# Optimization experiments

Hardware: AMD Instinct MI355X
Metric: run time of the kernel (lower is better)

## Reference

```python
import jax, jax.numpy as jnp
import numpy as np
from jax.scipy.special import logsumexp

GRID_N = 512
N_ITERS = 5


def _build_grid(n):
    nH = n * (n - 1)
    E = 2 * n * (n - 1)
    P = (n - 1) * (n - 1)
    N = n * n
    pi, pj = np.meshgrid(np.arange(n - 1), np.arange(n - 1), indexing='ij')
    pi, pj = pi.ravel(), pj.ravel()
    # child edges of plaquette (i,j): top/bottom horizontal, left/right vertical
    pce = np.stack([pi * (n - 1) + pj,
                    (pi + 1) * (n - 1) + pj,
                    nH + pi * n + pj,
                    nH + pi * n + pj + 1], 1).astype(np.int32)
    epp = np.zeros((E, 2), np.int32)
    eps = np.zeros((E, 2), np.int32)
    epm = np.zeros((E, 2), np.float32)
    ev = np.zeros((E, 2), np.int32)
    hi, hj = np.meshgrid(np.arange(n), np.arange(n - 1), indexing='ij')
    hi, hj = hi.ravel(), hj.ravel()
    he = hi * (n - 1) + hj
    m = hi < n - 1
    epp[he[m], 0] = hi[m] * (n - 1) + hj[m]; epm[he[m], 0] = 1; eps[he, 0] = 0
    m = hi > 0
    epp[he[m], 1] = (hi[m] - 1) * (n - 1) + hj[m]; epm[he[m], 1] = 1; eps[he, 1] = 1
    ev[he, 0] = hi * n + hj; ev[he, 1] = hi * n + hj + 1
    vi, vj = np.meshgrid(np.arange(n - 1), np.arange(n), indexing='ij')
    vi, vj = vi.ravel(), vj.ravel()
    ve = nH + vi * n + vj
    m = vj < n - 1
    epp[ve[m], 0] = vi[m] * (n - 1) + vj[m]; epm[ve[m], 0] = 1; eps[ve, 0] = 2
    m = vj > 0
    epp[ve[m], 1] = vi[m] * (n - 1) + vj[m] - 1; epm[ve[m], 1] = 1; eps[ve, 1] = 3
    ev[ve, 0] = vi * n + vj; ev[ve, 1] = (vi + 1) * n + vj
    return epp, eps, epm, pce, ev, E, P, N


def setup_inputs() -> dict:
    n = GRID_N
    epp, eps, epm, pce, ev, E, P, N = _build_grid(n)
    key = jax.random.key(0)
    k1, k2 = jax.random.split(key)
    return {
        'log_phi_plaq': 0.5 * jax.random.normal(k1, (P, 2, 2, 2, 2), jnp.float32),
        'log_phi_edge': 0.5 * jax.random.normal(k2, (E, 2, 2), jnp.float32),
        'edge_parent_plaq': jnp.asarray(epp),
        'edge_parent_slot': jnp.asarray(eps),
        'edge_parent_mask': jnp.asarray(epm),
        'plaq_child_edge': jnp.asarray(pce),
        'edge_vars': jnp.asarray(ev),
        'n_iters': N_ITERS,
        'n_vars': N,
    }


def _forward(log_phi_plaq, log_phi_edge, epp, eps, epm, pce, ev, n_iters, n_vars):
    P = log_phi_plaq.shape[0]
    maskNN = epm[:, :, None, None]

    def edge_totals(logM):
        # sum of log-messages from (<=2) parents into each edge, plus edge factor
        g = logM[epp, eps]                      # [E,2,2,2]
        return log_phi_edge + jnp.sum(g * maskNN, axis=1)  # [E,2,2]

    def plaq_terms(logM, tot):
        n_all = tot[pce] - logM                 # [P,4,2,2]: child msg excluding this parent
        b0 = n_all[:, 0, :, :, None, None]      # top edge -> vars (a,b)
        b1 = n_all[:, 1, None, None, :, :]      # bottom  -> vars (c,d)
        b2 = n_all[:, 2, :, None, :, None]      # left    -> vars (a,c)
        b3 = n_all[:, 3, None, :, None, :]      # right   -> vars (b,d)
        S = log_phi_plaq + b0 + b1 + b2 + b3    # [P,2,2,2,2] plaquette log-belief (unnorm)
        return S, (b0, b1, b2, b3)

    def step(logM, _):
        tot = edge_totals(logM)
        S, (b0, b1, b2, b3) = plaq_terms(logM, tot)
        m0 = logsumexp(S - b0, axis=(3, 4))
        m1 = logsumexp(S - b1, axis=(1, 2))
        m2 = logsumexp(S - b2, axis=(2, 4))
        m3 = logsumexp(S - b3, axis=(1, 3))
        new = jnp.stack([m0, m1, m2, m3], axis=1)
        new = new - logsumexp(new, axis=(2, 3), keepdims=True)  # normalize messages
        return new, None

    logM0 = jnp.full((P, 4, 2, 2), -jnp.log(4.0), log_phi_plaq.dtype)
    logM, _ = jax.lax.scan(step, logM0, None, length=n_iters)

    tot = edge_totals(logM)
    log_b_e = tot - logsumexp(tot, axis=(1, 2), keepdims=True)
    S, _ = plaq_terms(logM, tot)
    log_b_p = S - logsumexp(S, axis=(1, 2, 3, 4), keepdims=True)
    b_e = jnp.exp(log_b_e)
    b_p = jnp.exp(log_b_p)

    # Kikuchi free energy: c_plaq = 1, c_edge = 1 - #parents
    c_e = 1.0 - jnp.sum(epm, axis=1)
    F = (jnp.sum(b_p * (log_b_p - log_phi_plaq))
         + jnp.sum(c_e * jnp.sum(b_e * (log_b_e - log_phi_edge), axis=(1, 2))))

    binary_marginals = b_e                      # every pair is an R1 region
    pa = b_e.sum(axis=2)                        # [E,2] marginal of first var
    pb = b_e.sum(axis=1)                        # [E,2] marginal of second var
    ones = jnp.ones((ev.shape[0],), b_e.dtype)
    node_sum = (jax.ops.segment_sum(pa, ev[:, 0], num_segments=n_vars)
                + jax.ops.segment_sum(pb, ev[:, 1], num_segments=n_vars))
    deg = (jax.ops.segment_sum(ones, ev[:, 0], num_segments=n_vars)
           + jax.ops.segment_sum(ones, ev[:, 1], num_segments=n_vars))
    unary_marginals = node_sum / deg[:, None]   # [N,2]
    return -F, unary_marginals, binary_marginals


def reference(log_phi_plaq, log_phi_edge, edge_parent_plaq, edge_parent_slot,
              edge_parent_mask, plaq_child_edge, edge_vars, n_iters, n_vars):
    return _forward(log_phi_plaq, log_phi_edge, edge_parent_plaq, edge_parent_slot,
                    edge_parent_mask, plaq_child_edge, edge_vars, n_iters, n_vars)
```

## Files before the change

### kernel.cpp

```cpp
#include <hip/hip_runtime.h>
#include <hip/hip_fp16.h>
#include <math.h>


#define HALO  5
#define CORE  32
#define RW    (CORE + 2*HALO)
#define NCELL (RW*RW)
#define NTHR  512
#define QC    4
#define PHL_N 1536

static __device__ __forceinline__ float4 ld4(const float* p){ return *(const float4*)p; }
static __device__ __forceinline__ float rcpf(float x){ return __builtin_amdgcn_rcpf(x); }

static __device__ __forceinline__ void rd4(const __half2 (*pl)[2], int r, bool msk, float* o){
  __half2 a = pl[r][0], b = pl[r][1];
  float x0=__low2float(a), x1=__high2float(a), x2=__low2float(b), x3=__high2float(b);
  o[0]=msk?x0:1.f; o[1]=msk?x1:1.f; o[2]=msk?x2:1.f; o[3]=msk?x3:1.f;
}
static __device__ __forceinline__ void up4h(const __half2* p, int s, float* d){
  __half2 a = p[2*s], b = p[2*s+1];
  d[0]=__low2float(a); d[1]=__high2float(a); d[2]=__low2float(b); d[3]=__high2float(b);
}

__global__ __launch_bounds__(NTHR, 2)
void fused_kernel(const float* __restrict__ phiP, const float* __restrict__ phiE,
                  float* __restrict__ outBin, float* __restrict__ Pblk,
                  int m, int n)
{
  __shared__ __half2 pln[2][4][NCELL][2];
  __shared__ __half2 phL[8][PHL_N];
  const int t = threadIdx.x;
  const int base_i = (int)blockIdx.y*CORE - HALO;
  const int base_j = (int)blockIdx.x*CORE - HALO;
  const int nH = n*m;

  __half2 peH[QC][8], phH3[8];
  #pragma unroll
  for (int q=0; q<QC; ++q){
    const int r = t + q*NTHR;
    if (r < NCELL){
      const int ry = r / RW, rx = r - ry*RW;
      const int gi = base_i + ry, gj = base_j + rx;
      const int ci = min(max(gi,0), m-1), cj = min(max(gj,0), m-1);
      float4 v;
      v = ld4(phiE + 4*(size_t)(ci*m+cj));
      peH[q][0]=__floats2half2_rn(__expf(v.x),__expf(v.y));
      peH[q][1]=__floats2half2_rn(__expf(v.z),__expf(v.w));
      v = ld4(phiE + 4*(size_t)((ci+1)*m+cj));
      peH[q][2]=__floats2half2_rn(__expf(v.x),__expf(v.y));
      peH[q][3]=__floats2half2_rn(__expf(v.z),__expf(v.w));
      v = ld4(phiE + 4*(size_t)(nH+ci*n+cj));
      peH[q][4]=__floats2half2_rn(__expf(v.x),__expf(v.y));
      peH[q][5]=__floats2half2_rn(__expf(v.z),__expf(v.w));
      v = ld4(phiE + 4*(size_t)(nH+ci*n+cj+1));
      peH[q][6]=__floats2half2_rn(__expf(v.x),__expf(v.y));
      peH[q][7]=__floats2half2_rn(__expf(v.z),__expf(v.w));
      const float* pp = phiP + 16*(size_t)(ci*m+cj);
      #pragma unroll
      for (int h=0; h<4; ++h){
        v = ld4(pp + 4*h);
        __half2 h0 = __floats2half2_rn(__expf(v.x),__expf(v.y));
        __half2 h1 = __floats2half2_rn(__expf(v.z),__expf(v.w));
        if (q < 3){ phL[2*h+0][r] = h0; phL[2*h+1][r] = h1; }
        else      { phH3[2*h+0] = h0;  phH3[2*h+1] = h1; }
      }
    }
  }
  __syncthreads();

  for (int it=0; it<5; ++it){
    const int cb = it & 1, nb = cb ^ 1;
    #pragma unroll
    for (int q=0; q<QC; ++q){
      const int r = t + q*NTHR;
      if (r < NCELL){
        const int ry = r / RW, rx = r - ry*RW;
        const int gi = base_i + ry, gj = base_j + rx;
        const bool m0 = gi > 0, m1 = gi < m-1, m2 = gj > 0, m3 = gj < m-1;

        float pe[16];
        up4h(peH[q],0,pe+0); up4h(peH[q],1,pe+4);
        up4h(peH[q],2,pe+8); up4h(peH[q],3,pe+12);

        float na[4][4];
        if (it == 0){
          #pragma unroll
          for (int k=0;k<16;++k) na[k>>2][k&3] = pe[k];
        } else {
          const int r0 = max(ry-1,0)*RW + rx;
          const int r1 = min(ry+1,RW-1)*RW + rx;
          const int r2 = ry*RW + max(rx-1,0);
          const int r3 = ry*RW + min(rx+1,RW-1);
          float o[4];
          rd4(pln[cb][1], r0, m0, o);
          na[0][0]=pe[0]*o[0]; na[0][1]=pe[1]*o[1]; na[0][2]=pe[2]*o[2]; na[0][3]=pe[3]*o[3];
          rd4(pln[cb][0], r1, m1, o);
          na[1][0]=pe[4]*o[0]; na[1][1]=pe[5]*o[1]; na[1][2]=pe[6]*o[2]; na[1][3]=pe[7]*o[3];
          rd4(pln[cb][3], r2, m2, o);
          na[2][0]=pe[8]*o[0]; na[2][1]=pe[9]*o[1]; na[2][2]=pe[10]*o[2]; na[2][3]=pe[11]*o[3];
          rd4(pln[cb][2], r3, m3, o);
          na[3][0]=pe[12]*o[0]; na[3][1]=pe[13]*o[1]; na[3][2]=pe[14]*o[2]; na[3][3]=pe[15]*o[3];
        }

        float ph[16];
        if (q < 3){
          #pragma unroll
          for (int h=0; h<8; ++h){
            __half2 a = phL[h][r];
            ph[2*h]=__low2float(a); ph[2*h+1]=__high2float(a);
          }
        } else {
          up4h(phH3,0,ph+0); up4h(phH3,1,ph+4);
          up4h(phH3,2,ph+8); up4h(phH3,3,ph+12);
        }

        float g[4][4];
        #pragma unroll
        for (int s=0;s<4;++s){ g[s][0]=0.f; g[s][1]=0.f; g[s][2]=0.f; g[s][3]=0.f; }
        #pragma unroll
        for (int idx=0; idx<16; ++idx){
          const int a=(idx>>3)&1, b=(idx>>2)&1, c=(idx>>1)&1, d=idx&1;
          const int ab=(a<<1)|b, cd=(c<<1)|d, ac=(a<<1)|c, bd=(b<<1)|d;
          float E = (na[0][ab]*na[1][cd]) * (na[2][ac]*na[3][bd]) * ph[idx];
          g[0][ab]+=E; g[1][cd]+=E; g[2][ac]+=E; g[3][bd]+=E;
        }
        #pragma unroll
        for (int s=0;s<4;++s){
          float l1=na[s][0], l2=l1*na[s][1], l3=l2*na[s][2];
          float q2=na[s][3], q1=q2*na[s][2], q0=q1*na[s][1];
          float o0=g[s][0]*q0, o1=g[s][1]*l1*q1, o2=g[s][2]*l2*q2, o3=g[s][3]*l3;
          float inv = rcpf(fmaxf(fmaxf(o0,o1), fmaxf(o2,o3)));
          pln[nb][s][r][0] = __floats2half2_rn(o0*inv, o1*inv);
          pln[nb][s][r][1] = __floats2half2_rn(o2*inv, o3*inv);
        }
      }
    }
    __syncthreads();
  }

  float contrib = 0.f;
  #pragma unroll
  for (int q=0; q<QC; ++q){
    const int r = t + q*NTHR;
    if (r >= NCELL) continue;
    const int ry = r / RW, rx = r - ry*RW;
    const int gi = base_i + ry, gj = base_j + rx;
    const bool core = (ry >= HALO) && (ry < HALO+CORE) && (gi < m) &&
                      (rx >= HALO) && (rx < HALO+CORE) && (gj < m);
    if (!core) continue;
    const bool m0 = gi > 0, m1 = gi < m-1, m2 = gj > 0, m3 = gj < m-1;
    const int r0 = r - RW, r1 = r + RW, r2 = r - 1, r3 = r + 1;

    float pe[16], ph[16], own[16];
    up4h(peH[q],0,pe+0); up4h(peH[q],1,pe+4);
    up4h(peH[q],2,pe+8); up4h(peH[q],3,pe+12);
    if (q < 3){
      #pragma unroll
      for (int h=0; h<8; ++h){
        __half2 a = phL[h][r];
        ph[2*h]=__low2float(a); ph[2*h+1]=__high2float(a);
      }
    } else {
      up4h(phH3,0,ph+0); up4h(phH3,1,ph+4);
      up4h(phH3,2,ph+8); up4h(phH3,3,ph+12);
    }
    #pragma unroll
    for (int s=0;s<4;++s){
      __half2 a = pln[1][s][r][0], b = pln[1][s][r][1];
      own[4*s+0]=__low2float(a); own[4*s+1]=__high2float(a);
      own[4*s+2]=__low2float(b); own[4*s+3]=__high2float(b);
    }

    float o5_0[4], o5_2[4], na[4][4];
    {
      float o[4];
      rd4(pln[1][1], r0, m0, o5_0);
      na[0][0]=pe[0]*o5_0[0]; na[0][1]=pe[1]*o5_0[1];
      na[0][2]=pe[2]*o5_0[2]; na[0][3]=pe[3]*o5_0[3];
      rd4(pln[1][0], r1, m1, o);
      na[1][0]=pe[4]*o[0]; na[1][1]=pe[5]*o[1]; na[1][2]=pe[6]*o[2]; na[1][3]=pe[7]*o[3];
      rd4(pln[1][3], r2, m2, o5_2);
      na[2][0]=pe[8]*o5_2[0];  na[2][1]=pe[9]*o5_2[1];
      na[2][2]=pe[10]*o5_2[2]; na[2][3]=pe[11]*o5_2[3];
      rd4(pln[1][2], r3, m3, o);
      na[3][0]=pe[12]*o[0]; na[3][1]=pe[13]*o[1]; na[3][2]=pe[14]*o[2]; na[3][3]=pe[15]*o[3];
    }
    {
      float Ln[4][4];
      #pragma unroll
      for (int s=0;s<4;++s)
        #pragma unroll
        for (int k=0;k<4;++k)
          Ln[s][k] = __logf(fmaxf(na[s][k], 1e-30f));
      float Z=0.f, accT=0.f;
      #pragma unroll
      for (int idx=0; idx<16; ++idx){
        const int a=(idx>>3)&1, b=(idx>>2)&1, c=(idx>>1)&1, d=idx&1;
        const int ab=(a<<1)|b, cd=(c<<1)|d, ac=(a<<1)|c, bd=(b<<1)|d;
        float E = (na[0][ab]*na[1][cd]) * (na[2][ac]*na[3][bd]) * ph[idx];
        float T = (Ln[0][ab]+Ln[1][cd]) + (Ln[2][ac]+Ln[3][bd]);
        Z += E; accT = fmaf(E, T, accT);
      }
      contrib += accT*rcpf(Z) - __logf(Z);
    }
    {
      float P0=na[0][0]*own[0], P1=na[0][1]*own[1],
            P2=na[0][2]*own[2], P3=na[0][3]*own[3];
      float Zt=P0+P1+P2+P3, izt=rcpf(Zt);
      float* ob = outBin + 4*(size_t)(gi*m+gj);
      ob[0]=P0*izt; ob[1]=P1*izt; ob[2]=P2*izt; ob[3]=P3*izt;
      if (m0){
        float q0=__logf(fmaxf(o5_0[0]*own[0],1e-30f));
        float q1=__logf(fmaxf(o5_0[1]*own[1],1e-30f));
        float q2=__logf(fmaxf(o5_0[2]*own[2],1e-30f));
        float q3=__logf(fmaxf(o5_0[3]*own[3],1e-30f));
        contrib += __logf(Zt) - (P0*q0+P1*q1+P2*q2+P3*q3)*izt;
      }
    }
    {
      float P0=na[2][0]*own[8],  P1=na[2][1]*own[9],
            P2=na[2][2]*own[10], P3=na[2][3]*own[11];
      float Zt=P0+P1+P2+P3, izt=rcpf(Zt);
      float* ob = outBin + 4*(size_t)(nH+gi*n+gj);
      ob[0]=P0*izt; ob[1]=P1*izt; ob[2]=P2*izt; ob[3]=P3*izt;
      if (m2){
        float q0=__logf(fmaxf(o5_2[0]*own[8], 1e-30f));
        float q1=__logf(fmaxf(o5_2[1]*own[9], 1e-30f));
        float q2=__logf(fmaxf(o5_2[2]*own[10],1e-30f));
        float q3=__logf(fmaxf(o5_2[3]*own[11],1e-30f));
        contrib += __logf(Zt) - (P0*q0+P1*q1+P2*q2+P3*q3)*izt;
      }
    }
    if (gi == m-1){
      float P0=na[1][0]*own[4], P1=na[1][1]*own[5],
            P2=na[1][2]*own[6], P3=na[1][3]*own[7];
      float izt=rcpf(P0+P1+P2+P3);
      float* ob = outBin + 4*(size_t)((gi+1)*m+gj);
      ob[0]=P0*izt; ob[1]=P1*izt; ob[2]=P2*izt; ob[3]=P3*izt;
    }
    if (gj == m-1){
      float P0=na[3][0]*own[12], P1=na[3][1]*own[13],
            P2=na[3][2]*own[14], P3=na[3][3]*own[15];
      float izt=rcpf(P0+P1+P2+P3);
      float* ob = outBin + 4*(size_t)(nH+gi*n+gj+1);
      ob[0]=P0*izt; ob[1]=P1*izt; ob[2]=P2*izt; ob[3]=P3*izt;
    }
  }

  __syncthreads();
  float* red = (float*)&pln[0][0][0][0];
  #pragma unroll
  for (int off=32; off>0; off>>=1) contrib += __shfl_down(contrib, off, 64);
  if ((t & 63) == 0) red[t >> 6] = contrib;
  __syncthreads();
  if (t < 16){
    float v = (t < NTHR/64) ? red[t] : 0.f;
    #pragma unroll
    for (int off=8; off>0; off>>=1) v += __shfl_down(v, off, 16);
    if (t == 0) Pblk[blockIdx.y*gridDim.x + blockIdx.x] = v;
  }
}

__global__ __launch_bounds__(256)
void unary_kernel(const float* __restrict__ bin, float* __restrict__ out,
                  const float* __restrict__ Pblk, int m, int n, int nblk)
{
  if (blockIdx.x == 0 && blockIdx.y == 0){
    __shared__ float red[256];
    int tid = threadIdx.y*64 + threadIdx.x;
    float s = 0.f;
    for (int idx = tid; idx < nblk; idx += 256) s += Pblk[idx];
    red[tid] = s; __syncthreads();
    #pragma unroll
    for (int st=128; st>0; st>>=1){
      if (tid < st) red[tid] += red[tid+st];
      __syncthreads();
    }
    if (tid == 0) out[0] = -red[0];
  }
  int j = blockIdx.x*64 + threadIdx.x;
  int i = blockIdx.y*4  + threadIdx.y;
  if (i >= n || j >= n) return;
  const int nH = n*m;
  float s0=0.f, s1=0.f, deg=0.f;
  if (j < m){ const float* b = bin + 4*(size_t)(i*m+j);        s0 += b[0]+b[1]; s1 += b[2]+b[3]; deg+=1.f; }
  if (j > 0){ const float* b = bin + 4*(size_t)(i*m+j-1);      s0 += b[0]+b[2]; s1 += b[1]+b[3]; deg+=1.f; }
  if (i < m){ const float* b = bin + 4*(size_t)(nH+i*n+j);     s0 += b[0]+b[1]; s1 += b[2]+b[3]; deg+=1.f; }
  if (i > 0){ const float* b = bin + 4*(size_t)(nH+(i-1)*n+j); s0 += b[0]+b[2]; s1 += b[1]+b[3]; deg+=1.f; }
  float inv = 1.f/deg;
  size_t v = (size_t)i*n + j;
  out[1+2*v]   = s0*inv;
  out[1+2*v+1] = s1*inv;
}

extern "C" void kernel_launch(void* const* d_in, const int* in_sizes, int n_in,
                              void* d_out, int out_size, void* d_ws, size_t ws_size,
                              hipStream_t stream)
{
  const float* phiP = (const float*)d_in[0];
  const float* phiE = (const float*)d_in[1];
  int P  = in_sizes[0] / 16;
  int m  = (int)(sqrt((double)P) + 0.5);
  int n  = m + 1;
  int N  = n * n;
  float* out  = (float*)d_out;
  float* Pblk = (float*)d_ws;

  int tiles = (m + CORE - 1) / CORE;
  float* outBin = out + 1 + 2*(size_t)N;
  fused_kernel<<<dim3(tiles, tiles), dim3(NTHR), 0, stream>>>(phiP, phiE, outBin, Pblk, m, n);
  unary_kernel<<<dim3((n+63)/64, (n+3)/4), dim3(64,4), 0, stream>>>(outBin, out, Pblk, m, n, tiles*tiles);
}
```

Before: 125.8 us.

## Software-pipeline LDS neighbor loads and skip shrinking halo cells per iteration

Peels the first message-passing iteration, which needs no neighbor reads. Later iterations use a two-stage software pipeline that issues the shared-memory neighbor loads for the next cell group before computing the current one, hiding LDS latency. Cells inside the halo that can no longer affect the core region are skipped as iterations proceed, which cuts redundant work. The pipelining holds more values in registers, which may hurt occupancy under the 2-blocks launch bound.

```diff
diff --git a/kernel.cpp b/kernel.cpp
--- a/kernel.cpp
+++ b/kernel.cpp
@@ -23,6 +23,72 @@
   __half2 a = p[2*s], b = p[2*s+1];
   d[0]=__low2float(a); d[1]=__high2float(a); d[2]=__low2float(b); d[3]=__high2float(b);
 }
+
+#define ISSUE(q, S) do { \
+  const int r_ = t + (q)*NTHR; \
+  if (r_ < NCELL){ \
+    const int ry_ = r_ / RW, rx_ = r_ - ry_*RW; \
+    const int rr0 = max(ry_-1,0)*RW + rx_; \
+    const int rr1 = min(ry_+1,RW-1)*RW + rx_; \
+    const int rr2 = ry_*RW + max(rx_-1,0); \
+    const int rr3 = ry_*RW + min(rx_+1,RW-1); \
+    S[0][0]=pln[cb][1][rr0][0]; S[0][1]=pln[cb][1][rr0][1]; \
+    S[1][0]=pln[cb][0][rr1][0]; S[1][1]=pln[cb][0][rr1][1]; \
+    S[2][0]=pln[cb][3][rr2][0]; S[2][1]=pln[cb][3][rr2][1]; \
+    S[3][0]=pln[cb][2][rr3][0]; S[3][1]=pln[cb][2][rr3][1]; \
+  } } while(0)
+
+#define COMPUTE(q, S) do { \
+  const int r = t + (q)*NTHR; \
+  if (r < NCELL){ \
+    const int ry = r / RW, rx = r - ry*RW; \
+    if (ry>=it && ry<RW-it && rx>=it && rx<RW-it){ \
+      const int gi = base_i + ry, gj = base_j + rx; \
+      const bool m0 = gi > 0, m1 = gi < m-1, m2 = gj > 0, m3 = gj < m-1; \
+      float pe[16]; \
+      up4h(peH[q],0,pe+0); up4h(peH[q],1,pe+4); \
+      up4h(peH[q],2,pe+8); up4h(peH[q],3,pe+12); \
+      float na[4][4]; \
+      { float x0=__low2float(S[0][0]), x1=__high2float(S[0][0]), x2=__low2float(S[0][1]), x3=__high2float(S[0][1]); \
+        na[0][0]=pe[0]*(m0?x0:1.f); na[0][1]=pe[1]*(m0?x1:1.f); na[0][2]=pe[2]*(m0?x2:1.f); na[0][3]=pe[3]*(m0?x3:1.f); } \
+      { float x0=__low2float(S[1][0]), x1=__high2float(S[1][0]), x2=__low2float(S[1][1]), x3=__high2float(S[1][1]); \
+        na[1][0]=pe[4]*(m1?x0:1.f); na[1][1]=pe[5]*(m1?x1:1.f); na[1][2]=pe[6]*(m1?x2:1.f); na[1][3]=pe[7]*(m1?x3:1.f); } \
+      { float x0=__low2float(S[2][0]), x1=__high2float(S[2][0]), x2=__low2float(S[2][1]), x3=__high2float(S[2][1]); \
+        na[2][0]=pe[8]*(m2?x0:1.f); na[2][1]=pe[9]*(m2?x1:1.f); na[2][2]=pe[10]*(m2?x2:1.f); na[2][3]=pe[11]*(m2?x3:1.f); } \
+      { float x0=__low2float(S[3][0]), x1=__high2float(S[3][0]), x2=__low2float(S[3][1]), x3=__high2float(S[3][1]); \
+        na[3][0]=pe[12]*(m3?x0:1.f); na[3][1]=pe[13]*(m3?x1:1.f); na[3][2]=pe[14]*(m3?x2:1.f); na[3][3]=pe[15]*(m3?x3:1.f); } \
+      float ph[16]; \
+      if ((q) < 3){ \
+        _Pragma("unroll") \
+        for (int h=0; h<8; ++h){ \
+          __half2 a = phL[h][r]; \
+          ph[2*h]=__low2float(a); ph[2*h+1]=__high2float(a); \
+        } \
+      } else { \
+        up4h(phH3,0,ph+0); up4h(phH3,1,ph+4); \
+        up4h(phH3,2,ph+8); up4h(phH3,3,ph+12); \
+      } \
+      float g[4][4]; \
+      _Pragma("unroll") \
+      for (int s=0;s<4;++s){ g[s][0]=0.f; g[s][1]=0.f; g[s][2]=0.f; g[s][3]=0.f; } \
+      _Pragma("unroll") \
+      for (int idx=0; idx<16; ++idx){ \
+        const int a=(idx>>3)&1, b=(idx>>2)&1, c=(idx>>1)&1, d=idx&1; \
+        const int ab=(a<<1)|b, cd=(c<<1)|d, ac=(a<<1)|c, bd=(b<<1)|d; \
+        float E = (na[0][ab]*na[1][cd]) * (na[2][ac]*na[3][bd]) * ph[idx]; \
+        g[0][ab]+=E; g[1][cd]+=E; g[2][ac]+=E; g[3][bd]+=E; \
+      } \
+      _Pragma("unroll") \
+      for (int s=0;s<4;++s){ \
+        float l1=na[s][0], l2=l1*na[s][1], l3=l2*na[s][2]; \
+        float q2=na[s][3], q1=q2*na[s][2], q0=q1*na[s][1]; \
+        float o0=g[s][0]*q0, o1=g[s][1]*l1*q1, o2=g[s][2]*l2*q2, o3=g[s][3]*l3; \
+        float inv = rcpf(fmaxf(fmaxf(o0,o1), fmaxf(o2,o3))); \
+        pln[nb][s][r][0] = __floats2half2_rn(o0*inv, o1*inv); \
+        pln[nb][s][r][1] = __floats2half2_rn(o2*inv, o3*inv); \
+      } \
+    } \
+  } } while(0)
 
 __global__ __launch_bounds__(NTHR, 2)
 void fused_kernel(const float* __restrict__ phiP, const float* __restrict__ phiE,
@@ -70,40 +136,18 @@
   }
   __syncthreads();
 
-  for (int it=0; it<5; ++it){
-    const int cb = it & 1, nb = cb ^ 1;
+  {
+    const int nb = 1;
     #pragma unroll
     for (int q=0; q<QC; ++q){
       const int r = t + q*NTHR;
       if (r < NCELL){
-        const int ry = r / RW, rx = r - ry*RW;
-        const int gi = base_i + ry, gj = base_j + rx;
-        const bool m0 = gi > 0, m1 = gi < m-1, m2 = gj > 0, m3 = gj < m-1;
-
         float pe[16];
         up4h(peH[q],0,pe+0); up4h(peH[q],1,pe+4);
         up4h(peH[q],2,pe+8); up4h(peH[q],3,pe+12);
-
         float na[4][4];
-        if (it == 0){
-          #pragma unroll
-          for (int k=0;k<16;++k) na[k>>2][k&3] = pe[k];
-        } else {
-          const int r0 = max(ry-1,0)*RW + rx;
-          const int r1 = min(ry+1,RW-1)*RW + rx;
-          const int r2 = ry*RW + max(rx-1,0);
-          const int r3 = ry*RW + min(rx+1,RW-1);
-          float o[4];
-          rd4(pln[cb][1], r0, m0, o);
-          na[0][0]=pe[0]*o[0]; na[0][1]=pe[1]*o[1]; na[0][2]=pe[2]*o[2]; na[0][3]=pe[3]*o[3];
-          rd4(pln[cb][0], r1, m1, o);
-          na[1][0]=pe[4]*o[0]; na[1][1]=pe[5]*o[1]; na[1][2]=pe[6]*o[2]; na[1][3]=pe[7]*o[3];
-          rd4(pln[cb][3], r2, m2, o);
-          na[2][0]=pe[8]*o[0]; na[2][1]=pe[9]*o[1]; na[2][2]=pe[10]*o[2]; na[2][3]=pe[11]*o[3];
-          rd4(pln[cb][2], r3, m3, o);
-          na[3][0]=pe[12]*o[0]; na[3][1]=pe[13]*o[1]; na[3][2]=pe[14]*o[2]; na[3][3]=pe[15]*o[3];
-        }
-
+        #pragma unroll
+        for (int k=0;k<16;++k) na[k>>2][k&3] = pe[k];
         float ph[16];
         if (q < 3){
           #pragma unroll
@@ -115,7 +159,6 @@
           up4h(phH3,0,ph+0); up4h(phH3,1,ph+4);
           up4h(phH3,2,ph+8); up4h(phH3,3,ph+12);
         }
-
         float g[4][4];
         #pragma unroll
         for (int s=0;s<4;++s){ g[s][0]=0.f; g[s][1]=0.f; g[s][2]=0.f; g[s][3]=0.f; }
@@ -137,6 +180,18 @@
         }
       }
     }
+    __syncthreads();
+  }
+
+  for (int it=1; it<5; ++it){
+    const int cb = it & 1;
+    const int nb = cb ^ 1;
+    __half2 st0[4][2], st1[4][2];
+    ISSUE(0, st0);
+    ISSUE(1, st1);  COMPUTE(0, st0);
+    ISSUE(2, st0);  COMPUTE(1, st1);
+    ISSUE(3, st1);  COMPUTE(2, st0);
+    COMPUTE(3, st1);
     __syncthreads();
   }
 
```

New measurement: 125.6 us. Within noise of the previous version (-0.2%).

## Store pre-multiplied messages and run plaquette BP core in packed half2

Applied to the files above, without the earlier changes.

The loop now keeps messages in shared memory already multiplied by the edge potential, so the neighbour read directly gives the incoming belief. The 16-term plaquette marginalisation is computed with packed half2 multiplies and adds, and the exclusion products are replaced by reciprocals of the incoming values. A shrinking valid-halo check skips cells whose results are no longer needed at each iteration. The finalisation divides the edge potential back out to recover the plain messages. This cuts VALU work and conversions, at the cost of fp16 accumulation accuracy and possible underflow or overflow in half precision.

```diff
diff --git a/kernel.cpp b/kernel.cpp
--- a/kernel.cpp
+++ b/kernel.cpp
@@ -14,14 +14,59 @@
 static __device__ __forceinline__ float4 ld4(const float* p){ return *(const float4*)p; }
 static __device__ __forceinline__ float rcpf(float x){ return __builtin_amdgcn_rcpf(x); }
 
-static __device__ __forceinline__ void rd4(const __half2 (*pl)[2], int r, bool msk, float* o){
-  __half2 a = pl[r][0], b = pl[r][1];
-  float x0=__low2float(a), x1=__high2float(a), x2=__low2float(b), x3=__high2float(b);
-  o[0]=msk?x0:1.f; o[1]=msk?x1:1.f; o[2]=msk?x2:1.f; o[3]=msk?x3:1.f;
-}
 static __device__ __forceinline__ void up4h(const __half2* p, int s, float* d){
   __half2 a = p[2*s], b = p[2*s+1];
   d[0]=__low2float(a); d[1]=__high2float(a); d[2]=__low2float(b); d[3]=__high2float(b);
+}
+static __device__ __forceinline__ void rd4d(const __half2 (*pl)[2], int r, bool msk,
+                                            const float* dflt, float* o){
+  __half2 a = pl[r][0], b = pl[r][1];
+  float x0=__low2float(a), x1=__high2float(a), x2=__low2float(b), x3=__high2float(b);
+  o[0]=msk?x0:dflt[0]; o[1]=msk?x1:dflt[1]; o[2]=msk?x2:dflt[2]; o[3]=msk?x3:dflt[3];
+}
+
+static __device__ __forceinline__ void bp_core(const __half2* na8, const __half2* ph8,
+                                               __half2* g0p, __half2* g1p,
+                                               __half2* g2p, __half2* g3p)
+{
+  const __half2 hz = __floats2half2_rn(0.f, 0.f);
+  __half2 s0[4], s2[4];
+  s0[0]=__half2half2(__low2half(na8[0])); s0[1]=__half2half2(__high2half(na8[0]));
+  s0[2]=__half2half2(__low2half(na8[1])); s0[3]=__half2half2(__high2half(na8[1]));
+  s2[0]=__half2half2(__low2half(na8[4])); s2[1]=__half2half2(__high2half(na8[4]));
+  s2[2]=__half2half2(__low2half(na8[5])); s2[3]=__half2half2(__high2half(na8[5]));
+  __half2 n13[2][2];
+  n13[0][0]=__hmul2(na8[2],na8[6]); n13[0][1]=__hmul2(na8[3],na8[6]);
+  n13[1][0]=__hmul2(na8[2],na8[7]); n13[1][1]=__hmul2(na8[3],na8[7]);
+  g0p[0]=hz; g0p[1]=hz; g0p[2]=hz; g0p[3]=hz;
+  g2p[0]=hz; g2p[1]=hz; g2p[2]=hz; g2p[3]=hz;
+  g1p[0]=hz; g1p[1]=hz; g3p[0]=hz; g3p[1]=hz;
+  #pragma unroll
+  for (int a=0;a<2;++a)
+    #pragma unroll
+    for (int b=0;b<2;++b)
+      #pragma unroll
+      for (int c=0;c<2;++c){
+        const int ab=2*a+b, ac=2*a+c;
+        __half2 E = __hmul2(__hmul2(s0[ab],s2[ac]),
+                            __hmul2(n13[b][c], ph8[4*a+2*b+c]));
+        g0p[ab]=__hadd2(g0p[ab],E); g2p[ac]=__hadd2(g2p[ac],E);
+        g1p[c]=__hadd2(g1p[c],E);   g3p[b]=__hadd2(g3p[b],E);
+      }
+}
+
+static __device__ __forceinline__ void slot_out(float g0,float g1,float g2,float g3,
+                                                __half2 naA, __half2 naB,
+                                                __half2 peA, __half2 peB,
+                                                __half2* w0, __half2* w1)
+{
+  float2 nA = __half22float2(naA), nB = __half22float2(naB);
+  float r0=rcpf(fmaxf(nA.x,1e-30f)), r1=rcpf(fmaxf(nA.y,1e-30f));
+  float r2=rcpf(fmaxf(nB.x,1e-30f)), r3=rcpf(fmaxf(nB.y,1e-30f));
+  float o0=g0*r0, o1=g1*r1, o2=g2*r2, o3=g3*r3;
+  float inv = rcpf(fmaxf(fmaxf(o0,o1), fmaxf(o2,o3)));
+  *w0 = __hmul2(peA, __floats2half2_rn(o0*inv, o1*inv));
+  *w1 = __hmul2(peB, __floats2half2_rn(o2*inv, o3*inv));
 }
 
 __global__ __launch_bounds__(NTHR, 2)
@@ -77,63 +122,65 @@
       const int r = t + q*NTHR;
       if (r < NCELL){
         const int ry = r / RW, rx = r - ry*RW;
-        const int gi = base_i + ry, gj = base_j + rx;
-        const bool m0 = gi > 0, m1 = gi < m-1, m2 = gj > 0, m3 = gj < m-1;
-
-        float pe[16];
-        up4h(peH[q],0,pe+0); up4h(peH[q],1,pe+4);
-        up4h(peH[q],2,pe+8); up4h(peH[q],3,pe+12);
-
-        float na[4][4];
-        if (it == 0){
-          #pragma unroll
-          for (int k=0;k<16;++k) na[k>>2][k&3] = pe[k];
-        } else {
-          const int r0 = max(ry-1,0)*RW + rx;
-          const int r1 = min(ry+1,RW-1)*RW + rx;
-          const int r2 = ry*RW + max(rx-1,0);
-          const int r3 = ry*RW + min(rx+1,RW-1);
-          float o[4];
-          rd4(pln[cb][1], r0, m0, o);
-          na[0][0]=pe[0]*o[0]; na[0][1]=pe[1]*o[1]; na[0][2]=pe[2]*o[2]; na[0][3]=pe[3]*o[3];
-          rd4(pln[cb][0], r1, m1, o);
-          na[1][0]=pe[4]*o[0]; na[1][1]=pe[5]*o[1]; na[1][2]=pe[6]*o[2]; na[1][3]=pe[7]*o[3];
-          rd4(pln[cb][3], r2, m2, o);
-          na[2][0]=pe[8]*o[0]; na[2][1]=pe[9]*o[1]; na[2][2]=pe[10]*o[2]; na[2][3]=pe[11]*o[3];
-          rd4(pln[cb][2], r3, m3, o);
-          na[3][0]=pe[12]*o[0]; na[3][1]=pe[13]*o[1]; na[3][2]=pe[14]*o[2]; na[3][3]=pe[15]*o[3];
-        }
-
-        float ph[16];
-        if (q < 3){
-          #pragma unroll
-          for (int h=0; h<8; ++h){
-            __half2 a = phL[h][r];
-            ph[2*h]=__low2float(a); ph[2*h+1]=__high2float(a);
-          }
-        } else {
-          up4h(phH3,0,ph+0); up4h(phH3,1,ph+4);
-          up4h(phH3,2,ph+8); up4h(phH3,3,ph+12);
-        }
-
-        float g[4][4];
-        #pragma unroll
-        for (int s=0;s<4;++s){ g[s][0]=0.f; g[s][1]=0.f; g[s][2]=0.f; g[s][3]=0.f; }
-        #pragma unroll
-        for (int idx=0; idx<16; ++idx){
-          const int a=(idx>>3)&1, b=(idx>>2)&1, c=(idx>>1)&1, d=idx&1;
-          const int ab=(a<<1)|b, cd=(c<<1)|d, ac=(a<<1)|c, bd=(b<<1)|d;
-          float E = (na[0][ab]*na[1][cd]) * (na[2][ac]*na[3][bd]) * ph[idx];
-          g[0][ab]+=E; g[1][cd]+=E; g[2][ac]+=E; g[3][bd]+=E;
-        }
-        #pragma unroll
-        for (int s=0;s<4;++s){
-          float l1=na[s][0], l2=l1*na[s][1], l3=l2*na[s][2];
-          float q2=na[s][3], q1=q2*na[s][2], q0=q1*na[s][1];
-          float o0=g[s][0]*q0, o1=g[s][1]*l1*q1, o2=g[s][2]*l2*q2, o3=g[s][3]*l3;
-          float inv = rcpf(fmaxf(fmaxf(o0,o1), fmaxf(o2,o3)));
-          pln[nb][s][r][0] = __floats2half2_rn(o0*inv, o1*inv);
-          pln[nb][s][r][1] = __floats2half2_rn(o2*inv, o3*inv);
+        if (ry>=it && ry<RW-it && rx>=it && rx<RW-it){
+          const int gi = base_i + ry, gj = base_j + rx;
+
+          __half2 na8[8];
+          if (it == 0){
+            #pragma unroll
+            for (int h=0; h<8; ++h) na8[h] = peH[q][h];
+          } else {
+            const bool m0 = gi > 0, m1 = gi < m-1, m2 = gj > 0, m3 = gj < m-1;
+            const int r0 = r-RW, r1 = r+RW, r2 = r-1, r3 = r+1;
+            na8[0] = m0 ? pln[cb][1][r0][0] : peH[q][0];
+            na8[1] = m0 ? pln[cb][1][r0][1] : peH[q][1];
+            na8[2] = m1 ? pln[cb][0][r1][0] : peH[q][2];
+            na8[3] = m1 ? pln[cb][0][r1][1] : peH[q][3];
+            na8[4] = m2 ? pln[cb][3][r2][0] : peH[q][4];
+            na8[5] = m2 ? pln[cb][3][r2][1] : peH[q][5];
+            na8[6] = m3 ? pln[cb][2][r3][0] : peH[q][6];
+            na8[7] = m3 ? pln[cb][2][r3][1] : peH[q][7];
+          }
+
+          __half2 ph8[8];
+          if (q < 3){
+            #pragma unroll
+            for (int h=0; h<8; ++h) ph8[h] = phL[h][r];
+          } else {
+            #pragma unroll
+            for (int h=0; h<8; ++h) ph8[h] = phH3[h];
+          }
+
+          __half2 g0p[4], g1p[2], g2p[4], g3p[2];
+          bp_core(na8, ph8, g0p, g1p, g2p, g3p);
+
+          __half2 w0, w1;
+          {
+            float2 a0=__half22float2(g0p[0]), a1=__half22float2(g0p[1]);
+            float2 a2=__half22float2(g0p[2]), a3=__half22float2(g0p[3]);
+            slot_out(a0.x+a0.y, a1.x+a1.y, a2.x+a2.y, a3.x+a3.y,
+                     na8[0], na8[1], peH[q][0], peH[q][1], &w0, &w1);
+            pln[nb][0][r][0]=w0; pln[nb][0][r][1]=w1;
+          }
+          {
+            float2 a=__half22float2(g1p[0]), b=__half22float2(g1p[1]);
+            slot_out(a.x, a.y, b.x, b.y,
+                     na8[2], na8[3], peH[q][2], peH[q][3], &w0, &w1);
+            pln[nb][1][r][0]=w0; pln[nb][1][r][1]=w1;
+          }
+          {
+            float2 a0=__half22float2(g2p[0]), a1=__half22float2(g2p[1]);
+            float2 a2=__half22float2(g2p[2]), a3=__half22float2(g2p[3]);
+            slot_out(a0.x+a0.y, a1.x+a1.y, a2.x+a2.y, a3.x+a3.y,
+                     na8[4], na8[5], peH[q][4], peH[q][5], &w0, &w1);
+            pln[nb][2][r][0]=w0; pln[nb][2][r][1]=w1;
+          }
+          {
+            float2 a=__half22float2(g3p[0]), b=__half22float2(g3p[1]);
+            slot_out(a.x, a.y, b.x, b.y,
+                     na8[6], na8[7], peH[q][6], peH[q][7], &w0, &w1);
+            pln[nb][3][r][0]=w0; pln[nb][3][r][1]=w1;
+          }
         }
       }
     }
@@ -153,7 +200,7 @@
     const bool m0 = gi > 0, m1 = gi < m-1, m2 = gj > 0, m3 = gj < m-1;
     const int r0 = r - RW, r1 = r + RW, r2 = r - 1, r3 = r + 1;
 
-    float pe[16], ph[16], own[16];
+    float pe[16], ph[16], ownM[16];
     up4h(peH[q],0,pe+0); up4h(peH[q],1,pe+4);
     up4h(peH[q],2,pe+8); up4h(peH[q],3,pe+12);
     if (q < 3){
@@ -169,80 +216,68 @@
     #pragma unroll
     for (int s=0;s<4;++s){
       __half2 a = pln[1][s][r][0], b = pln[1][s][r][1];
-      own[4*s+0]=__low2float(a); own[4*s+1]=__high2float(a);
-      own[4*s+2]=__low2float(b); own[4*s+3]=__high2float(b);
-    }
-
-    float o5_0[4], o5_2[4], na[4][4];
-    {
-      float o[4];
-      rd4(pln[1][1], r0, m0, o5_0);
-      na[0][0]=pe[0]*o5_0[0]; na[0][1]=pe[1]*o5_0[1];
-      na[0][2]=pe[2]*o5_0[2]; na[0][3]=pe[3]*o5_0[3];
-      rd4(pln[1][0], r1, m1, o);
-      na[1][0]=pe[4]*o[0]; na[1][1]=pe[5]*o[1]; na[1][2]=pe[6]*o[2]; na[1][3]=pe[7]*o[3];
-      rd4(pln[1][3], r2, m2, o5_2);
-      na[2][0]=pe[8]*o5_2[0];  na[2][1]=pe[9]*o5_2[1];
-      na[2][2]=pe[10]*o5_2[2]; na[2][3]=pe[11]*o5_2[3];
-      rd4(pln[1][2], r3, m3, o);
-      na[3][0]=pe[12]*o[0]; na[3][1]=pe[13]*o[1]; na[3][2]=pe[14]*o[2]; na[3][3]=pe[15]*o[3];
-    }
+      ownM[4*s+0]=__low2float(a); ownM[4*s+1]=__high2float(a);
+      ownM[4*s+2]=__low2float(b); ownM[4*s+3]=__high2float(b);
+    }
+
+    float naf[4][4];
+    rd4d(pln[1][1], r0, m0, pe+0,  naf[0]);
+    rd4d(pln[1][0], r1, m1, pe+4,  naf[1]);
+    rd4d(pln[1][3], r2, m2, pe+8,  naf[2]);
+    rd4d(pln[1][2], r3, m3, pe+12, naf[3]);
+
     {
       float Ln[4][4];
       #pragma unroll
       for (int s=0;s<4;++s)
         #pragma unroll
         for (int k=0;k<4;++k)
-          Ln[s][k] = __logf(fmaxf(na[s][k], 1e-30f));
+          Ln[s][k] = __logf(fmaxf(naf[s][k], 1e-30f));
       float Z=0.f, accT=0.f;
       #pragma unroll
       for (int idx=0; idx<16; ++idx){
         const int a=(idx>>3)&1, b=(idx>>2)&1, c=(idx>>1)&1, d=idx&1;
         const int ab=(a<<1)|b, cd=(c<<1)|d, ac=(a<<1)|c, bd=(b<<1)|d;
-        float E = (na[0][ab]*na[1][cd]) * (na[2][ac]*na[3][bd]) * ph[idx];
+        float E = (naf[0][ab]*naf[1][cd]) * (naf[2][ac]*naf[3][bd]) * ph[idx];
         float T = (Ln[0][ab]+Ln[1][cd]) + (Ln[2][ac]+Ln[3][bd]);
         Z += E; accT = fmaf(E, T, accT);
       }
       contrib += accT*rcpf(Z) - __logf(Z);
     }
     {
-      float P0=na[0][0]*own[0], P1=na[0][1]*own[1],
-            P2=na[0][2]*own[2], P3=na[0][3]*own[3];
+      float rp0=rcpf(pe[0]), rp1=rcpf(pe[1]), rp2=rcpf(pe[2]), rp3=rcpf(pe[3]);
+      float P0=naf[0][0]*ownM[0]*rp0, P1=naf[0][1]*ownM[1]*rp1,
+            P2=naf[0][2]*ownM[2]*rp2, P3=naf[0][3]*ownM[3]*rp3;
       float Zt=P0+P1+P2+P3, izt=rcpf(Zt);
       float* ob = outBin + 4*(size_t)(gi*m+gj);
       ob[0]=P0*izt; ob[1]=P1*izt; ob[2]=P2*izt; ob[3]=P3*izt;
       if (m0){
-        float q0=__logf(fmaxf(o5_0[0]*own[0],1e-30f));
-        float q1=__logf(fmaxf(o5_0[1]*own[1],1e-30f));
-        float q2=__logf(fmaxf(o5_0[2]*own[2],1e-30f));
-        float q3=__logf(fmaxf(o5_0[3]*own[3],1e-30f));
+        float q0=__logf(fmaxf(P0*rp0,1e-30f)), q1=__logf(fmaxf(P1*rp1,1e-30f));
+        float q2=__logf(fmaxf(P2*rp2,1e-30f)), q3=__logf(fmaxf(P3*rp3,1e-30f));
         contrib += __logf(Zt) - (P0*q0+P1*q1+P2*q2+P3*q3)*izt;
       }
     }
     {
-      float P0=na[2][0]*own[8],  P1=na[2][1]*own[9],
-            P2=na[2][2]*own[10], P3=na[2][3]*own[11];
+      float rp0=rcpf(pe[8]), rp1=rcpf(pe[9]), rp2=rcpf(pe[10]), rp3=rcpf(pe[11]);
+      float P0=naf[2][0]*ownM[8]*rp0,  P1=naf[2][1]*ownM[9]*rp1,
+            P2=naf[2][2]*ownM[10]*rp2, P3=naf[2][3]*ownM[11]*rp3;
       float Zt=P0+P1+P2+P3, izt=rcpf(Zt);
       float* ob = outBin + 4*(size_t)(nH+gi*n+gj);
       ob[0]=P0*izt; ob[1]=P1*izt; ob[2]=P2*izt; ob[3]=P3*izt;
       if (m2){
-        float q0=__logf(fmaxf(o5_2[0]*own[8], 1e-30f));
-        float q1=__logf(fmaxf(o5_2[1]*own[9], 1e-30f));
-        float q2=__logf(fmaxf(o5_2[2]*own[10],1e-30f));
-        float q3=__logf(fmaxf(o5_2[3]*own[11],1e-30f));
+        float q0=__logf(fmaxf(P0*rp0,1e-30f)), q1=__logf(fmaxf(P1*rp1,1e-30f));
+        float q2=__logf(fmaxf(P2*rp2,1e-30f)), q3=__logf(fmaxf(P3*rp3,1e-30f));
         contrib += __logf(Zt) - (P0*q0+P1*q1+P2*q2+P3*q3)*izt;
       }
     }
     if (gi == m-1){
-      float P0=na[1][0]*own[4], P1=na[1][1]*own[5],
-            P2=na[1][2]*own[6], P3=na[1][3]*own[7];
+      float P0=ownM[4], P1=ownM[5], P2=ownM[6], P3=ownM[7];
       float izt=rcpf(P0+P1+P2+P3);
       float* ob = outBin + 4*(size_t)((gi+1)*m+gj);
       ob[0]=P0*izt; ob[1]=P1*izt; ob[2]=P2*izt; ob[3]=P3*izt;
     }
     if (gj == m-1){
-      float P0=na[3][0]*own[12], P1=na[3][1]*own[13],
-            P2=na[3][2]*own[14], P3=na[3][3]*own[15];
+      float P0=ownM[12], P1=ownM[13], P2=ownM[14], P3=ownM[15];
       float izt=rcpf(P0+P1+P2+P3);
       float* ob = outBin + 4*(size_t)(nH+gi*n+gj+1);
       ob[0]=P0*izt; ob[1]=P1*izt; ob[2]=P2*izt; ob[3]=P3*izt;
```

New measurement: 124.5 us. About the same (-1.1%).
